# Optimization experiments

Measured on AMD Instinct MI355X. Metric: run time of the kernel, lower is better.

## Reference

```python
import jax, jax.numpy as jnp
import numpy as np

# Lattice gauge L-CNN convolution (eq. 5 of arXiv:2012.12901), real-valued analogue.
B, L, D, KK, N_IN, N_OUT, NC = 2, 16, 4, 2, 8, 8, 3  # batch, side, dirs, kernel reach, channels, SU(3)


def setup_inputs() -> dict:
    key = jax.random.key(0)
    kW, kU, kO = jax.random.split(key, 3)
    # W: locally transforming variables, (batch, L1..L4, N_in, Nc, Nc)
    W = jax.random.normal(kW, (B, L, L, L, L, N_IN, NC, NC), dtype=jnp.float32)
    # U_PT: parallel transporters, (batch, L1..L4, d, 2K+1, Nc, Nc)
    U_PT = jax.random.normal(kU, (B, L, L, L, L, D, 2 * KK + 1, NC, NC), dtype=jnp.float32)
    # omega: conv coefficients, (N_out, N_in, d, 2K+1)
    omega = jax.random.normal(kO, (N_OUT, N_IN, D, 2 * KK + 1), dtype=jnp.float32) * 0.1
    return {"W": W, "U_PT": U_PT, "omega": omega}


def _apply_L_conv(W, U_PT, omega):
    """Gauge-equivariant lattice conv: shift + parallel-transport sandwich + accumulate.

    W:     (b, L1..Ld, N_in, Nc, Nc)
    U_PT:  (b, L1..Ld, d, 2K+1, Nc, Nc)
    omega: (N_out, N_in, d, 2K+1)
    returns (b, L1..Ld, N_out, Nc, Nc)
    """
    K = (U_PT.shape[-3] - 1) // 2
    d = U_PT.shape[-4]
    N_out = omega.shape[0]
    out = jnp.zeros(W.shape[:-3] + (N_out,) + W.shape[-2:], dtype=W.dtype)
    for k in range(-K, K + 1):          # fixed small kernel-offset loop
        i_k = k + K
        for mu in range(d):             # fixed small direction loop
            W_shift = jnp.roll(W, shift=-k, axis=1 + mu)
            U = U_PT[..., mu, i_k, :, :]  # (b, lattice, Nc, Nc)
            # torch: einsum('ij,...ac,...jcd,...db->...iab', om, U, Ws, U.adjoint())
            # real adjoint = transpose: (U^T)_{db} = U_{bd}
            out = out + jnp.einsum(
                'ij,...ac,...jcd,...bd->...iab',
                omega[..., mu, i_k], U, W_shift, U)
    return out


def reference(W, U_PT, omega):
    return _apply_L_conv(W, U_PT, omega)
```

## Files before the change

### kernel.cpp

```cpp
#include <hip/hip_runtime.h>

#define NSITES (2 * 16 * 16 * 16 * 16)

#define OM_OFF 0
#define U_OFF  1312
#define LDS_FLOATS (U_OFF + 5888)

#define DO_CH(T, w0,w1,w2,w3,w4,w5,w6,w7,w8) do {                           \
    float M[9];                                                             \
    _Pragma("unroll")                                                       \
    for (int a = 0; a < 3; ++a) {                                           \
        const float uw0 = fmaf(U[a*3+0], (w0),                              \
                          fmaf(U[a*3+1], (w3), U[a*3+2] * (w6)));           \
        const float uw1 = fmaf(U[a*3+0], (w1),                              \
                          fmaf(U[a*3+1], (w4), U[a*3+2] * (w7)));           \
        const float uw2 = fmaf(U[a*3+0], (w2),                              \
                          fmaf(U[a*3+1], (w5), U[a*3+2] * (w8)));           \
        _Pragma("unroll")                                                   \
        for (int b2 = 0; b2 < 3; ++b2)                                      \
            M[a*3+b2] = fmaf(uw0, U[b2*3+0],                                \
                        fmaf(uw1, U[b2*3+1], uw2 * U[b2*3+2]));             \
    }                                                                       \
    const float4 wo = *reinterpret_cast<const float4*>(                     \
                          omt + ik * 64 + jown8 + (T) * 8);                 \
    const float4 wp = *reinterpret_cast<const float4*>(                     \
                          omt + ik * 64 + jpar8 + (T) * 8);                 \
    const float wov[4] = {wo.x, wo.y, wo.z, wo.w};                          \
    const float wpv[4] = {wp.x, wp.y, wp.z, wp.w};                          \
    _Pragma("unroll")                                                       \
    for (int e = 0; e < 9; ++e) {                                           \
        const float mp = __shfl_xor(M[e], 4);                               \
        _Pragma("unroll")                                                   \
        for (int ii = 0; ii < 4; ++ii)                                      \
            acc[ii][e] = fmaf(wov[ii], M[e], fmaf(wpv[ii], mp, acc[ii][e]));\
    }                                                                       \
} while (0)

__global__ __launch_bounds__(256, 8) void lconv_kernel(
    const float* __restrict__ W, const float* __restrict__ U_PT,
    const float* __restrict__ omega, float* __restrict__ out)
{
    __shared__ float lds[LDS_FLOATS];
    const int tid = threadIdx.x;

    const int bid = ((int)blockIdx.x & 7) * ((int)gridDim.x >> 3)
                  + ((int)blockIdx.x >> 3);
    const int s0  = bid * 32;

    {
        const int site = tid >> 3;
        const int r8   = tid & 7;

        for (int t = tid; t < 1280; t += 256) {
            const int i  = t / 160;
            const int r  = t - i * 160;
            const int j  = r / 20;
            const int r2 = r - j * 20;
            const int m  = r2 / 5;
            const int ik = r2 - m * 5;
            lds[OM_OFF + m * 328 + ik * 64 + j * 8 + i] = omega[t];
        }

        const float4* __restrict__ U4 =
            reinterpret_cast<const float4*>(U_PT) + (size_t)s0 * 45;
#pragma unroll
        for (int st = 0; st < 6; ++st) {
            const int f4r = st * 8 + r8;
            if (st < 5 || f4r < 45) {
                *reinterpret_cast<float4*>(
                    lds + U_OFF + site * 184 + f4r * 4) =
                    U4[site * 45 + f4r];
            }
        }
    }
    __syncthreads();

    const int local = tid >> 3;
    const int s     = s0 + local;
    const int jh    = (tid >> 2) & 1;
    const int mu    = tid & 3;
    const int sh    = 12 - 4 * mu;
    const int x     = (s >> sh) & 15;

    const float* __restrict__ Ul  = lds + U_OFF + local * 184 + mu * 45;
    const float* __restrict__ omt = lds + OM_OFF + mu * 328 + jh * 4;
    const int jown8 = jh * 32;
    const int jpar8 = (jh ^ 1) * 32;

    float acc[4][9];
#pragma unroll
    for (int i = 0; i < 4; ++i)
#pragma unroll
        for (int e = 0; e < 9; ++e) acc[i][e] = 0.0f;

#pragma unroll 1
    for (int ik = 0; ik < 5; ++ik) {
        const int k = ik - 2;

        const int ns = s + ((((x + k + 16) & 15) - x) << sh);
        const float4* __restrict__ Wp =
            reinterpret_cast<const float4*>(W + (size_t)ns * 72 + jh * 36);

        float U[9];
#pragma unroll
        for (int e = 0; e < 9; ++e) U[e] = Ul[ik * 9 + e];

        {
            const float4 a0 = Wp[0], a1 = Wp[1], a2 = Wp[2];
            DO_CH(0, a0.x, a0.y, a0.z, a0.w, a1.x, a1.y, a1.z, a1.w, a2.x);
            const float4 a3 = Wp[3], a4 = Wp[4];
            DO_CH(1, a2.y, a2.z, a2.w, a3.x, a3.y, a3.z, a3.w, a4.x, a4.y);
            const float4 a5 = Wp[5], a6 = Wp[6];
            DO_CH(2, a4.z, a4.w, a5.x, a5.y, a5.z, a5.w, a6.x, a6.y, a6.z);
            const float4 a7 = Wp[7], a8 = Wp[8];
            DO_CH(3, a6.w, a7.x, a7.y, a7.z, a7.w, a8.x, a8.y, a8.z, a8.w);
        }
    }

#pragma unroll
    for (int i = 0; i < 4; ++i)
#pragma unroll
        for (int e = 0; e < 9; ++e) {
            float v = acc[i][e];
            v += __shfl_xor(v, 1);
            v += __shfl_xor(v, 2);
            acc[i][e] = v;
        }

    if (mu == 0) {
        float4* __restrict__ o4 =
            reinterpret_cast<float4*>(out + (size_t)s * 72 + jh * 36);
#pragma unroll
        for (int q = 0; q < 9; ++q) {
            const int f = q * 4;
            o4[q] = make_float4(acc[(f + 0) / 9][(f + 0) % 9],
                                acc[(f + 1) / 9][(f + 1) % 9],
                                acc[(f + 2) / 9][(f + 2) % 9],
                                acc[(f + 3) / 9][(f + 3) % 9]);
        }
    }
}

extern "C" void kernel_launch(void* const* d_in, const int* in_sizes, int n_in,
                              void* d_out, int out_size, void* d_ws, size_t ws_size,
                              hipStream_t stream) {
    const float* W   = (const float*)d_in[0];
    const float* U   = (const float*)d_in[1];
    const float* om  = (const float*)d_in[2];
    float*       out = (float*)d_out;

    const int block = 256;
    const int grid  = NSITES / 32;
    hipLaunchKernelGGL(lconv_kernel, dim3(grid), dim3(block), 0, stream,
                       W, U, om, out);
}
```

Before: 109.9 us.

## Pre-transpose W into site-major float4 planes for coalesced gathers

Adds a transpose kernel that rewrites W from site-major (72 floats per site) into 18 float4 planes indexed by site, staged in the workspace. The conv kernel then reads each float4 plane with a stride of NSITES, so adjacent threads load adjacent sites instead of 288-byte-strided records. It also drops the occupancy hint from launch_bounds. In exchange it costs an extra kernel launch plus a full read and write of W (about 38 MB) every call, and it falls back to the old path when the workspace is too small.

New measurement: 123.8 us. +12.6%, slower.

```diff
diff --git a/kernel.cpp b/kernel.cpp
--- a/kernel.cpp
+++ b/kernel.cpp
@@ -1,6 +1,6 @@
 #include <hip/hip_runtime.h>
 
-#define NSITES (2 * 16 * 16 * 16 * 16)
+#define NSITES (1 << 17)
 
 #define OM_OFF 0
 #define U_OFF  1312
@@ -36,8 +36,36 @@
     }                                                                       \
 } while (0)
 
-__global__ __launch_bounds__(256, 8) void lconv_kernel(
-    const float* __restrict__ W, const float* __restrict__ U_PT,
+__global__ __launch_bounds__(256) void transpose_w(
+    const float4* __restrict__ W4, float4* __restrict__ WT4)
+{
+    __shared__ float4 tile[18 * 65];
+    const int t  = threadIdx.x;
+    const int s0 = (int)blockIdx.x * 64;
+#pragma unroll
+    for (int p = 0; p < 5; ++p) {
+        const int f = p * 256 + t;
+        if (f < 1152) {
+            const int sl = f / 18;
+            const int q  = f - sl * 18;
+            tile[q * 65 + sl] = W4[(size_t)s0 * 18 + f];
+        }
+    }
+    __syncthreads();
+#pragma unroll
+    for (int p = 0; p < 5; ++p) {
+        const int g = p * 256 + t;
+        if (g < 1152) {
+            const int q  = g >> 6;
+            const int sl = g & 63;
+            WT4[(size_t)q * NSITES + s0 + sl] = tile[q * 65 + sl];
+        }
+    }
+}
+
+template <bool TR>
+__global__ __launch_bounds__(256) void lconv_kernel(
+    const float* __restrict__ Wsrc, const float* __restrict__ U_PT,
     const float* __restrict__ omega, float* __restrict__ out)
 {
     __shared__ float lds[LDS_FLOATS];
@@ -87,6 +115,9 @@
     const int jown8 = jh * 32;
     const int jpar8 = (jh ^ 1) * 32;
 
+    const float4* __restrict__ Wt4 = reinterpret_cast<const float4*>(Wsrc);
+    const int     jh9NS            = jh * 9 * NSITES;
+
     float acc[4][9];
 #pragma unroll
     for (int i = 0; i < 4; ++i)
@@ -98,21 +129,25 @@
         const int k = ik - 2;
 
         const int ns = s + ((((x + k + 16) & 15) - x) << sh);
-        const float4* __restrict__ Wp =
-            reinterpret_cast<const float4*>(W + (size_t)ns * 72 + jh * 36);
 
         float U[9];
 #pragma unroll
         for (int e = 0; e < 9; ++e) U[e] = Ul[ik * 9 + e];
 
+        const float4* __restrict__ Wb;
+        if constexpr (TR) Wb = Wt4 + ((size_t)jh9NS + ns);
+        else              Wb = reinterpret_cast<const float4*>(
+                                   Wsrc + (size_t)ns * 72 + jh * 36);
+        constexpr int STR = TR ? NSITES : 1;
+
         {
-            const float4 a0 = Wp[0], a1 = Wp[1], a2 = Wp[2];
+            const float4 a0 = Wb[0*STR], a1 = Wb[1*STR], a2 = Wb[2*STR];
             DO_CH(0, a0.x, a0.y, a0.z, a0.w, a1.x, a1.y, a1.z, a1.w, a2.x);
-            const float4 a3 = Wp[3], a4 = Wp[4];
+            const float4 a3 = Wb[3*STR], a4 = Wb[4*STR];
             DO_CH(1, a2.y, a2.z, a2.w, a3.x, a3.y, a3.z, a3.w, a4.x, a4.y);
-            const float4 a5 = Wp[5], a6 = Wp[6];
+            const float4 a5 = Wb[5*STR], a6 = Wb[6*STR];
             DO_CH(2, a4.z, a4.w, a5.x, a5.y, a5.z, a5.w, a6.x, a6.y, a6.z);
-            const float4 a7 = Wp[7], a8 = Wp[8];
+            const float4 a7 = Wb[7*STR], a8 = Wb[8*STR];
             DO_CH(3, a6.w, a7.x, a7.y, a7.z, a7.w, a8.x, a8.y, a8.z, a8.w);
         }
     }
@@ -149,8 +184,15 @@
     const float* om  = (const float*)d_in[2];
     float*       out = (float*)d_out;
 
-    const int block = 256;
-    const int grid  = NSITES / 32;
-    hipLaunchKernelGGL(lconv_kernel, dim3(grid), dim3(block), 0, stream,
-                       W, U, om, out);
+    const size_t wt_bytes = (size_t)18 * NSITES * 16;
+
+    if (ws_size >= wt_bytes) {
+        transpose_w<<<NSITES / 64, 256, 0, stream>>>(
+            (const float4*)W, (float4*)d_ws);
+        lconv_kernel<true><<<NSITES / 32, 256, 0, stream>>>(
+            (const float*)d_ws, U, om, out);
+    } else {
+        lconv_kernel<false><<<NSITES / 32, 256, 0, stream>>>(
+            W, U, om, out);
+    }
 }
```

## Mix input channels with omega before the sandwich, split outputs across 16 lanes per site

Applied to the files above, without the earlier changes.

Because U W U^T is linear in W, the omega channel mixing now happens first: each thread forms two output-channel combinations of all eight input W matrices, then applies one U·V·U^T sandwich per output channel instead of one per input channel. This cuts the sandwich work and removes the cross-lane shuffle used for channel mixing. Each site now gets 16 threads (4 directions × 4 output pairs) and blocks cover 16 sites, so grid size doubles. The cost is that every thread loads the full 72-float W row, which raises global/L2 load traffic per thread.

New measurement: 266.9 us. 143% more time.

```diff
diff --git a/kernel.cpp b/kernel.cpp
--- a/kernel.cpp
+++ b/kernel.cpp
@@ -1,39 +1,39 @@
 #include <hip/hip_runtime.h>
 
-#define NSITES (2 * 16 * 16 * 16 * 16)
+#define NSITES (1 << 17)
 
 #define OM_OFF 0
 #define U_OFF  1312
-#define LDS_FLOATS (U_OFF + 5888)
+#define LDS_FLOATS (U_OFF + 16 * 184)
 
-#define DO_CH(T, w0,w1,w2,w3,w4,w5,w6,w7,w8) do {                           \
-    float M[9];                                                             \
-    _Pragma("unroll")                                                       \
-    for (int a = 0; a < 3; ++a) {                                           \
-        const float uw0 = fmaf(U[a*3+0], (w0),                              \
-                          fmaf(U[a*3+1], (w3), U[a*3+2] * (w6)));           \
-        const float uw1 = fmaf(U[a*3+0], (w1),                              \
-                          fmaf(U[a*3+1], (w4), U[a*3+2] * (w7)));           \
-        const float uw2 = fmaf(U[a*3+0], (w2),                              \
-                          fmaf(U[a*3+1], (w5), U[a*3+2] * (w8)));           \
-        _Pragma("unroll")                                                   \
-        for (int b2 = 0; b2 < 3; ++b2)                                      \
-            M[a*3+b2] = fmaf(uw0, U[b2*3+0],                                \
-                        fmaf(uw1, U[b2*3+1], uw2 * U[b2*3+2]));             \
-    }                                                                       \
-    const float4 wo = *reinterpret_cast<const float4*>(                     \
-                          omt + ik * 64 + jown8 + (T) * 8);                 \
-    const float4 wp = *reinterpret_cast<const float4*>(                     \
-                          omt + ik * 64 + jpar8 + (T) * 8);                 \
-    const float wov[4] = {wo.x, wo.y, wo.z, wo.w};                          \
-    const float wpv[4] = {wp.x, wp.y, wp.z, wp.w};                          \
-    _Pragma("unroll")                                                       \
-    for (int e = 0; e < 9; ++e) {                                           \
-        const float mp = __shfl_xor(M[e], 4);                               \
-        _Pragma("unroll")                                                   \
-        for (int ii = 0; ii < 4; ++ii)                                      \
-            acc[ii][e] = fmaf(wov[ii], M[e], fmaf(wpv[ii], mp, acc[ii][e]));\
-    }                                                                       \
+#define MIX_CH(FIRST, J, w0,w1,w2,w3,w4,w5,w6,w7,w8) do {                    \
+    const float2 o2 = *reinterpret_cast<const float2*>(                      \
+                          omt + ik * 64 + (J) * 8);                          \
+    const float wv[9] = {w0,w1,w2,w3,w4,w5,w6,w7,w8};                        \
+    _Pragma("unroll")                                                        \
+    for (int e = 0; e < 9; ++e) {                                            \
+        if (FIRST) { V0[e] = o2.x * wv[e];                                   \
+                     V1[e] = o2.y * wv[e]; }                                 \
+        else       { V0[e] = fmaf(o2.x, wv[e], V0[e]);                       \
+                     V1[e] = fmaf(o2.y, wv[e], V1[e]); }                     \
+    }                                                                        \
+} while (0)
+
+#define SAND(Vv, av) do {                                                    \
+    _Pragma("unroll")                                                        \
+    for (int a = 0; a < 3; ++a) {                                            \
+        const float uw0 = fmaf(U[a*3+0], Vv[0],                              \
+                          fmaf(U[a*3+1], Vv[3], U[a*3+2] * Vv[6]));          \
+        const float uw1 = fmaf(U[a*3+0], Vv[1],                              \
+                          fmaf(U[a*3+1], Vv[4], U[a*3+2] * Vv[7]));          \
+        const float uw2 = fmaf(U[a*3+0], Vv[2],                              \
+                          fmaf(U[a*3+1], Vv[5], U[a*3+2] * Vv[8]));          \
+        _Pragma("unroll")                                                    \
+        for (int b = 0; b < 3; ++b)                                          \
+            av[a*3+b] = fmaf(uw0, U[b*3+0],                                  \
+                        fmaf(uw1, U[b*3+1],                                  \
+                        fmaf(uw2, U[b*3+2], av[a*3+b])));                    \
+    }                                                                        \
 } while (0)
 
 __global__ __launch_bounds__(256, 8) void lconv_kernel(
@@ -45,28 +45,26 @@
 
     const int bid = ((int)blockIdx.x & 7) * ((int)gridDim.x >> 3)
                   + ((int)blockIdx.x >> 3);
-    const int s0  = bid * 32;
+    const int s0  = bid * 16;
 
     {
-        const int site = tid >> 3;
-        const int r8   = tid & 7;
-
         for (int t = tid; t < 1280; t += 256) {
             const int i  = t / 160;
             const int r  = t - i * 160;
             const int j  = r / 20;
             const int r2 = r - j * 20;
             const int m  = r2 / 5;
-            const int ik = r2 - m * 5;
-            lds[OM_OFF + m * 328 + ik * 64 + j * 8 + i] = omega[t];
+            const int ikk = r2 - m * 5;
+            lds[OM_OFF + m * 328 + ikk * 64 + j * 8 + i] = omega[t];
         }
-
+        const int site = tid >> 4;
+        const int r16  = tid & 15;
         const float4* __restrict__ U4 =
             reinterpret_cast<const float4*>(U_PT) + (size_t)s0 * 45;
 #pragma unroll
-        for (int st = 0; st < 6; ++st) {
-            const int f4r = st * 8 + r8;
-            if (st < 5 || f4r < 45) {
+        for (int st = 0; st < 3; ++st) {
+            const int f4r = st * 16 + r16;
+            if (st < 2 || f4r < 45) {
                 *reinterpret_cast<float4*>(
                     lds + U_OFF + site * 184 + f4r * 4) =
                     U4[site * 45 + f4r];
@@ -75,23 +73,19 @@
     }
     __syncthreads();
 
-    const int local = tid >> 3;
+    const int local = tid >> 4;
     const int s     = s0 + local;
-    const int jh    = (tid >> 2) & 1;
+    const int q     = (tid >> 2) & 3;
     const int mu    = tid & 3;
     const int sh    = 12 - 4 * mu;
     const int x     = (s >> sh) & 15;
 
     const float* __restrict__ Ul  = lds + U_OFF + local * 184 + mu * 45;
-    const float* __restrict__ omt = lds + OM_OFF + mu * 328 + jh * 4;
-    const int jown8 = jh * 32;
-    const int jpar8 = (jh ^ 1) * 32;
+    const float* __restrict__ omt = lds + OM_OFF + mu * 328 + q * 2;
 
-    float acc[4][9];
+    float acc0[9], acc1[9];
 #pragma unroll
-    for (int i = 0; i < 4; ++i)
-#pragma unroll
-        for (int e = 0; e < 9; ++e) acc[i][e] = 0.0f;
+    for (int e = 0; e < 9; ++e) { acc0[e] = 0.0f; acc1[e] = 0.0f; }
 
 #pragma unroll 1
     for (int ik = 0; ik < 5; ++ik) {
@@ -99,45 +93,60 @@
 
         const int ns = s + ((((x + k + 16) & 15) - x) << sh);
         const float4* __restrict__ Wp =
-            reinterpret_cast<const float4*>(W + (size_t)ns * 72 + jh * 36);
+            reinterpret_cast<const float4*>(W + (size_t)ns * 72);
+
+        float V0[9], V1[9];
+        {
+            const float4 a0 = Wp[0], a1 = Wp[1], a2 = Wp[2];
+            MIX_CH(1, 0, a0.x,a0.y,a0.z,a0.w, a1.x,a1.y,a1.z,a1.w, a2.x);
+            const float4 a3 = Wp[3], a4 = Wp[4];
+            MIX_CH(0, 1, a2.y,a2.z,a2.w, a3.x,a3.y,a3.z,a3.w, a4.x,a4.y);
+            const float4 a5 = Wp[5], a6 = Wp[6];
+            MIX_CH(0, 2, a4.z,a4.w, a5.x,a5.y,a5.z,a5.w, a6.x,a6.y,a6.z);
+            const float4 a7 = Wp[7], a8 = Wp[8];
+            MIX_CH(0, 3, a6.w, a7.x,a7.y,a7.z,a7.w, a8.x,a8.y,a8.z,a8.w);
+            const float4 a9 = Wp[9], a10 = Wp[10], a11 = Wp[11];
+            MIX_CH(0, 4, a9.x,a9.y,a9.z,a9.w, a10.x,a10.y,a10.z,a10.w, a11.x);
+            const float4 a12 = Wp[12], a13 = Wp[13];
+            MIX_CH(0, 5, a11.y,a11.z,a11.w, a12.x,a12.y,a12.z,a12.w, a13.x,a13.y);
+            const float4 a14 = Wp[14], a15 = Wp[15];
+            MIX_CH(0, 6, a13.z,a13.w, a14.x,a14.y,a14.z,a14.w, a15.x,a15.y,a15.z);
+            const float4 a16 = Wp[16], a17 = Wp[17];
+            MIX_CH(0, 7, a15.w, a16.x,a16.y,a16.z,a16.w, a17.x,a17.y,a17.z,a17.w);
+        }
 
         float U[9];
 #pragma unroll
         for (int e = 0; e < 9; ++e) U[e] = Ul[ik * 9 + e];
 
-        {
-            const float4 a0 = Wp[0], a1 = Wp[1], a2 = Wp[2];
-            DO_CH(0, a0.x, a0.y, a0.z, a0.w, a1.x, a1.y, a1.z, a1.w, a2.x);
-            const float4 a3 = Wp[3], a4 = Wp[4];
-            DO_CH(1, a2.y, a2.z, a2.w, a3.x, a3.y, a3.z, a3.w, a4.x, a4.y);
-            const float4 a5 = Wp[5], a6 = Wp[6];
-            DO_CH(2, a4.z, a4.w, a5.x, a5.y, a5.z, a5.w, a6.x, a6.y, a6.z);
-            const float4 a7 = Wp[7], a8 = Wp[8];
-            DO_CH(3, a6.w, a7.x, a7.y, a7.z, a7.w, a8.x, a8.y, a8.z, a8.w);
-        }
+        SAND(V0, acc0);
+        SAND(V1, acc1);
     }
 
 #pragma unroll
-    for (int i = 0; i < 4; ++i)
-#pragma unroll
-        for (int e = 0; e < 9; ++e) {
-            float v = acc[i][e];
-            v += __shfl_xor(v, 1);
-            v += __shfl_xor(v, 2);
-            acc[i][e] = v;
-        }
+    for (int e = 0; e < 9; ++e) {
+        float v0 = acc0[e];
+        v0 += __shfl_xor(v0, 1);
+        v0 += __shfl_xor(v0, 2);
+        acc0[e] = v0;
+        float v1 = acc1[e];
+        v1 += __shfl_xor(v1, 1);
+        v1 += __shfl_xor(v1, 2);
+        acc1[e] = v1;
+    }
 
     if (mu == 0) {
-        float4* __restrict__ o4 =
-            reinterpret_cast<float4*>(out + (size_t)s * 72 + jh * 36);
-#pragma unroll
-        for (int q = 0; q < 9; ++q) {
-            const int f = q * 4;
-            o4[q] = make_float4(acc[(f + 0) / 9][(f + 0) % 9],
-                                acc[(f + 1) / 9][(f + 1) % 9],
-                                acc[(f + 2) / 9][(f + 2) % 9],
-                                acc[(f + 3) / 9][(f + 3) % 9]);
-        }
+        float2* __restrict__ o2 =
+            reinterpret_cast<float2*>(out + (size_t)s * 72 + q * 18);
+        o2[0] = make_float2(acc0[0], acc0[1]);
+        o2[1] = make_float2(acc0[2], acc0[3]);
+        o2[2] = make_float2(acc0[4], acc0[5]);
+        o2[3] = make_float2(acc0[6], acc0[7]);
+        o2[4] = make_float2(acc0[8], acc1[0]);
+        o2[5] = make_float2(acc1[1], acc1[2]);
+        o2[6] = make_float2(acc1[3], acc1[4]);
+        o2[7] = make_float2(acc1[5], acc1[6]);
+        o2[8] = make_float2(acc1[7], acc1[8]);
     }
 }
 
@@ -150,7 +159,7 @@
     float*       out = (float*)d_out;
 
     const int block = 256;
-    const int grid  = NSITES / 32;
+    const int grid  = NSITES / 16;
     hipLaunchKernelGGL(lconv_kernel, dim3(grid), dim3(block), 0, stream,
                        W, U, om, out);
 }
```
